# Optimization experiments

Hardware: AMD Instinct MI355X
Metric: run time of the kernel (lower is better)

## Reference

```python
import jax, jax.numpy as jnp
import numpy as np


def setup_inputs() -> dict:
    key = jax.random.key(0)
    kq, kk, kv = jax.random.split(key, 3)
    d_head, sq, skv = 128, 8192, 8192
    q = jax.random.normal(kq, (d_head, sq), dtype=jnp.float32)
    k = jax.random.normal(kk, (d_head, skv), dtype=jnp.float32)
    v = jax.random.normal(kv, (d_head, skv), dtype=jnp.float32)
    return {"q": q, "k": k, "v": v}


def reference(q, k, v):
    # qk: (seqlen_q, seqlen_kv) -- full score matrix, no 1/sqrt(d) scaling (faithful)
    qk = jnp.einsum('dq,dk->qk', q, k)
    row_max = jnp.max(qk, axis=1, keepdims=True)
    exp_row = jnp.exp(qk - row_max)
    scores = exp_row / jnp.sum(exp_row, axis=1, keepdims=True)
    # attn_out: (seqlen_q, d_head)
    attn_out = jnp.einsum('qk,dk->qd', scores, v)
    return attn_out
```

## Files before the change

### kernel.cpp

```cpp
#include <hip/hip_runtime.h>
#include <hip/hip_bf16.h>
#include <math.h>

typedef _Float16 half8 __attribute__((ext_vector_type(8)));
typedef __fp16 fp16x2 __attribute__((ext_vector_type(2)));
typedef float f32x4 __attribute__((ext_vector_type(4)));
typedef float f32x16 __attribute__((ext_vector_type(16)));
typedef unsigned uint4v __attribute__((ext_vector_type(4)));

#define D 128
#define SQ 8192
#define SKV 8192
#define BQ 256
#define BKV 64
#define LOG2E 1.4426950408889634f
#define DEFER_THR 11.5417f

__device__ __forceinline__ float bf2f(ushort h) {
  union { unsigned u; float f; } v; v.u = ((unsigned)h) << 16;
  return v.f;
}
__device__ __forceinline__ unsigned cvtpk_bf(float a, float b) {
  unsigned r;
  asm("v_cvt_pk_bf16_f32 %0, %1, %2" : "=v"(r) : "v"(a), "v"(b));
  return r;
}
__device__ __forceinline__ unsigned cvtpk_h(float a, float b) {
  union { fp16x2 h; unsigned u; } r;
  r.h = __builtin_amdgcn_cvt_pkrtz(a, b);
  return r.u;
}
__device__ __forceinline__ float fexp2(float x) {
  float r;
  asm("v_exp_f32 %0, %1" : "=v"(r) : "v"(x));
  return r;
}
__device__ __forceinline__ float fmax3(float a, float b, float c) {
  float r;
  asm("v_max3_f32 %0, %1, %2, %3" : "=v"(r) : "v"(a), "v"(b), "v"(c));
  return r;
}
__device__ __forceinline__ void pl32swap(unsigned& a, unsigned& b) {
  asm("v_permlane32_swap_b32 %0, %1" : "+v"(a), "+v"(b));
}

__global__ void prep_all(const float* __restrict__ q, const float* __restrict__ k,
                         const float* __restrict__ v,
                         _Float16* __restrict__ QT, _Float16* __restrict__ PK,
                         _Float16* __restrict__ PV) {
  int b = blockIdx.x;
  int t = threadIdx.x;
  if (b < 512) {
    const bool isQ = (b < 256);
    const float* src = isQ ? q : k;
    const float scl = isQ ? LOG2E : 1.0f;
    int s0 = (isQ ? b : b - 256) * 32;
    __shared__ float lds[128][33];
    int dr = t >> 5, l = t & 31;
#pragma unroll
    for (int j = 0; j < 16; ++j) {
      int dd = dr * 16 + j;
      lds[dd][l] = src[(size_t)dd * SQ + s0 + l];
    }
    __syncthreads();
#pragma unroll
    for (int i = 0; i < 2; ++i) {
      int cid = t + i * 256;
      int c = cid >> 5, sl = cid & 31;
      half8 hv;
#pragma unroll
      for (int e = 0; e < 8; ++e) hv[e] = (_Float16)(lds[c * 8 + e][sl] * scl);
      if (isQ) {
        *(half8*)(QT + (size_t)(s0 + sl) * D + c * 8) = hv;
      } else {
        int srow = s0 + sl;
        size_t elem = (size_t)((srow >> 5) * 8 + (c >> 1)) * 512 +
                      ((c & 1) * 32 + (srow & 31)) * 8;
        *(half8*)(PK + elem) = hv;
      }
    }
  } else {
    int idx = (b - 512) * 256 + t;
    int i8 = idx * 8;
    float4 x0 = *(const float4*)(v + i8);
    float4 x1 = *(const float4*)(v + i8 + 4);
    int drow = i8 >> 13;
    int kv = i8 & (SKV - 1);
    size_t elem = (size_t)(kv >> 6) * 8192 +
                  (size_t)((drow >> 5) * 4 + ((kv >> 4) & 3)) * 512 +
                  (((kv >> 3) & 1) * 32 + (drow & 31)) * 8;
    half8 hv = { (_Float16)x0.x, (_Float16)x0.y, (_Float16)x0.z, (_Float16)x0.w,
                 (_Float16)x1.x, (_Float16)x1.y, (_Float16)x1.z, (_Float16)x1.w };
    *(half8*)(PV + elem) = hv;
  }
}

__global__ __launch_bounds__(512, 2)
void flash_fwd(const _Float16* __restrict__ QT, const _Float16* __restrict__ PK,
               const _Float16* __restrict__ PV,
               ushort* __restrict__ Opart, float* __restrict__ Mst,
               float* __restrict__ Lst, int splitLen) {
  __shared__ _Float16 Kl[2][BKV * D];
  __shared__ _Float16 Vl[3][BKV * D];

  const int tid = threadIdx.x;
  const int w = tid >> 6;
  const int lane = tid & 63;
  const int lc = lane & 31;
  const int hi = lane >> 5;
  const int qb = blockIdx.x;
  const int split = blockIdx.y;
  const int qrow = qb * BQ + w * 32 + lc;

  half8 qh[8];
#pragma unroll
  for (int ds = 0; ds < 8; ++ds)
    qh[ds] = *(const half8*)(QT + (size_t)qrow * D + ds * 16 + hi * 8);

  f32x16 Ot[4];
#pragma unroll
  for (int dt = 0; dt < 4; ++dt)
#pragma unroll
    for (int e = 0; e < 16; ++e) Ot[dt][e] = 0.f;
  float mrun = -INFINITY, lrun = 0.f;

  const int kvBase = split * splitLen;
  const int nsteps = splitLen / BKV;
  const int tB = kvBase / BKV;

#define STAGE(KB, VB, T)                                                      \
  {                                                                           \
    _Pragma("unroll")                                                         \
    for (int j = 0; j < 4; ++j) {                                             \
      int cblk = w * 4 + j;                                                   \
      int cc = cblk & 15;                                                     \
      const _Float16* gp = ((cblk < 16) ? PK : PV) +                          \
                           (size_t)(T) * (BKV * D) + cc * 512 + lane * 8;     \
      _Float16* lp = ((cblk < 16) ? &Kl[KB][0] : &Vl[VB][0]) + cc * 512;      \
      __builtin_amdgcn_global_load_lds(                                       \
          (const __attribute__((address_space(1))) unsigned*)gp,              \
          (__attribute__((address_space(3))) unsigned*)lp, 16, 0, 0);         \
    }                                                                         \
  }

  auto QKX = [&](int kb2, f32x16& s0, f32x16& s1) {
    const _Float16* kb = &Kl[kb2][0] + lane * 8;
#pragma unroll
    for (int e = 0; e < 16; ++e) { s0[e] = 0.f; s1[e] = 0.f; }
    __builtin_amdgcn_s_setprio(1);
#pragma unroll
    for (int ds = 0; ds < 8; ++ds) {
      half8 k0 = *(const half8*)(kb + ds * 512);
      half8 k1 = *(const half8*)(kb + (8 + ds) * 512);
      s0 = __builtin_amdgcn_mfma_f32_32x32x16_f16(k0, qh[ds], s0, 0, 0, 0);
      s1 = __builtin_amdgcn_mfma_f32_32x32x16_f16(k1, qh[ds], s1, 0, 0, 0);
    }
    __builtin_amdgcn_s_setprio(0);
  };

  auto SMPV = [&](f32x16& s0, f32x16& s1, int vb3) {
    const _Float16* vb = &Vl[vb3][0] + lane * 8;
    half8 va[16];
#pragma unroll
    for (int f = 0; f < 16; ++f) va[f] = *(const half8*)(vb + f * 512);

    float m0 = fmax3(s0[0], s0[1], s0[2]);
    float m1 = fmax3(s0[3], s0[4], s0[5]);
    float m2 = fmax3(s0[6], s0[7], s0[8]);
    float m3 = fmax3(s0[9], s0[10], s0[11]);
    float m4 = fmax3(s0[12], s0[13], s0[14]);
    float m5 = fmax3(s0[15], s1[0], s1[1]);
    float m6 = fmax3(s1[2], s1[3], s1[4]);
    float m7 = fmax3(s1[5], s1[6], s1[7]);
    float m8 = fmax3(s1[8], s1[9], s1[10]);
    float m9 = fmax3(s1[11], s1[12], s1[13]);
    float ma = fmaxf(s1[14], s1[15]);
    float n0 = fmax3(m0, m1, m2);
    float n1 = fmax3(m3, m4, m5);
    float n2 = fmax3(m6, m7, m8);
    float n3 = fmaxf(m9, ma);
    float mx = fmaxf(fmax3(n0, n1, n2), n3);
    mx = fmaxf(mx, __shfl_xor(mx, 32));

    if (!__all(mx - mrun <= DEFER_THR)) {
      float mn = fmaxf(mrun, mx);
      float sc = fexp2(mrun - mn);
      mrun = mn;
      lrun *= sc;
#pragma unroll
      for (int dt = 0; dt < 4; ++dt)
#pragma unroll
        for (int e = 0; e < 16; ++e) Ot[dt][e] *= sc;
    }
#pragma unroll
    for (int e = 0; e < 16; ++e) {
      s0[e] = fexp2(s0[e] - mrun);
      s1[e] = fexp2(s1[e] - mrun);
    }
    float a8[8];
#pragma unroll
    for (int e = 0; e < 8; ++e) a8[e] = (s0[e] + s0[e + 8]) + (s1[e] + s1[e + 8]);
    float lsum = ((a8[0] + a8[4]) + (a8[1] + a8[5])) +
                 ((a8[2] + a8[6]) + (a8[3] + a8[7]));
    lsum += __shfl_xor(lsum, 32);
    lrun += lsum;

    unsigned pk[8];
    half8 pb[4];
    union { unsigned u[4]; half8 v; } pbu;
#pragma unroll
    for (int j = 0; j < 8; ++j) pk[j] = cvtpk_h(s0[2 * j], s0[2 * j + 1]);
    pl32swap(pk[0], pk[2]); pl32swap(pk[1], pk[3]);
    pl32swap(pk[4], pk[6]); pl32swap(pk[5], pk[7]);
    pbu.u[0] = pk[0]; pbu.u[1] = pk[1]; pbu.u[2] = pk[2]; pbu.u[3] = pk[3]; pb[0] = pbu.v;
    pbu.u[0] = pk[4]; pbu.u[1] = pk[5]; pbu.u[2] = pk[6]; pbu.u[3] = pk[7]; pb[1] = pbu.v;
#pragma unroll
    for (int j = 0; j < 8; ++j) pk[j] = cvtpk_h(s1[2 * j], s1[2 * j + 1]);
    pl32swap(pk[0], pk[2]); pl32swap(pk[1], pk[3]);
    pl32swap(pk[4], pk[6]); pl32swap(pk[5], pk[7]);
    pbu.u[0] = pk[0]; pbu.u[1] = pk[1]; pbu.u[2] = pk[2]; pbu.u[3] = pk[3]; pb[2] = pbu.v;
    pbu.u[0] = pk[4]; pbu.u[1] = pk[5]; pbu.u[2] = pk[6]; pbu.u[3] = pk[7]; pb[3] = pbu.v;

    __builtin_amdgcn_s_setprio(1);
#pragma unroll
    for (int dt = 0; dt < 4; ++dt) {
      Ot[dt] = __builtin_amdgcn_mfma_f32_32x32x16_f16(va[dt * 4 + 0], pb[0], Ot[dt], 0, 0, 0);
      Ot[dt] = __builtin_amdgcn_mfma_f32_32x32x16_f16(va[dt * 4 + 1], pb[1], Ot[dt], 0, 0, 0);
      Ot[dt] = __builtin_amdgcn_mfma_f32_32x32x16_f16(va[dt * 4 + 2], pb[2], Ot[dt], 0, 0, 0);
      Ot[dt] = __builtin_amdgcn_mfma_f32_32x32x16_f16(va[dt * 4 + 3], pb[3], Ot[dt], 0, 0, 0);
    }
    __builtin_amdgcn_s_setprio(0);
  };

  f32x16 sA0, sA1, sB0, sB1;

  STAGE(0, 0, tB);
  __syncthreads();
  if (nsteps > 1) STAGE(1, 1, tB + 1);
  QKX(0, sA0, sA1);
  __syncthreads();

  int p = 1;
  for (; p + 1 < nsteps; p += 2) {
    STAGE(0, (p + 1) % 3, tB + p + 1);
    QKX(1, sB0, sB1);
    SMPV(sA0, sA1, (p - 1) % 3);
    __syncthreads();
    if (p + 2 < nsteps) STAGE(1, (p + 2) % 3, tB + p + 2);
    QKX(0, sA0, sA1);
    SMPV(sB0, sB1, p % 3);
    __syncthreads();
  }
  if (p < nsteps) {
    QKX(1, sB0, sB1);
    SMPV(sA0, sA1, (p - 1) % 3);
    SMPV(sB0, sB1, p % 3);
  } else {
    SMPV(sA0, sA1, (nsteps - 1) % 3);
  }

  ushort* Op = Opart + (size_t)split * SQ * D + (size_t)qrow * D;
#pragma unroll
  for (int dt = 0; dt < 4; ++dt) {
#pragma unroll
    for (int rg = 0; rg < 4; ++rg) {
      uint2 o2;
      o2.x = cvtpk_bf(Ot[dt][4 * rg + 0], Ot[dt][4 * rg + 1]);
      o2.y = cvtpk_bf(Ot[dt][4 * rg + 2], Ot[dt][4 * rg + 3]);
      *(uint2*)(Op + dt * 32 + rg * 8 + hi * 4) = o2;
    }
  }
  if (hi == 0) {
    Mst[split * SQ + qrow] = mrun;
    Lst[split * SQ + qrow] = lrun;
  }
}

__global__ void combine(const ushort* __restrict__ Opart, const float* __restrict__ Mst,
                        const float* __restrict__ Lst, float* __restrict__ out, int nsplit) {
  int t8 = (blockIdx.x * 256 + threadIdx.x) * 8;
  int qi = t8 >> 7;
  float M = -INFINITY;
  for (int s = 0; s < nsplit; ++s) M = fmaxf(M, Mst[s * SQ + qi]);
  float acc[8] = {0.f, 0.f, 0.f, 0.f, 0.f, 0.f, 0.f, 0.f};
  float den = 0.f;
  for (int s = 0; s < nsplit; ++s) {
    float wgt = fexp2(Mst[s * SQ + qi] - M);
    den += wgt * Lst[s * SQ + qi];
    uint4v u = *(const uint4v*)(Opart + (size_t)s * SQ * D + t8);
#pragma unroll
    for (int j = 0; j < 4; ++j) {
      acc[2 * j]     += wgt * bf2f((ushort)(u[j] & 0xffffu));
      acc[2 * j + 1] += wgt * bf2f((ushort)(u[j] >> 16));
    }
  }
  float inv = 1.0f / den;
  f32x4 o0 = { acc[0] * inv, acc[1] * inv, acc[2] * inv, acc[3] * inv };
  f32x4 o1 = { acc[4] * inv, acc[5] * inv, acc[6] * inv, acc[7] * inv };
  *(f32x4*)(out + t8) = o0;
  *(f32x4*)(out + t8 + 4) = o1;
}

extern "C" void kernel_launch(void* const* d_in, const int* in_sizes, int n_in,
                              void* d_out, int out_size, void* d_ws, size_t ws_size,
                              hipStream_t stream) {
  const float* q = (const float*)d_in[0];
  const float* k = (const float*)d_in[1];
  const float* v = (const float*)d_in[2];
  float* out = (float*)d_out;

  char* ws = (char*)d_ws;
  const size_t mat = (size_t)SQ * D * 2;
  _Float16* QT = (_Float16*)(ws);
  _Float16* PK = (_Float16*)(ws + mat);
  _Float16* PV = (_Float16*)(ws + 2 * mat);
  char* rest = ws + 3 * mat;

  const size_t opartSz = (size_t)SQ * D * 2;
  const size_t statSz  = (size_t)SQ * 4;
  int nsplit = 8;
  while (nsplit > 1 &&
         3 * mat + (size_t)nsplit * (opartSz + 2 * statSz) > ws_size) nsplit >>= 1;

  ushort* Opart = (ushort*)rest;
  float* Mst = (float*)(rest + (size_t)nsplit * opartSz);
  float* Lst = (float*)(rest + (size_t)nsplit * opartSz + (size_t)nsplit * statSz);

  prep_all<<<1024, 256, 0, stream>>>(q, k, v, QT, PK, PV);
  flash_fwd<<<dim3(SQ / BQ, nsplit), 512, 0, stream>>>(QT, PK, PV,
                                                       Opart, Mst, Lst, SKV / nsplit);
  combine<<<(SQ * D) / (256 * 8), 256, 0, stream>>>(Opart, Mst, Lst, out, nsplit);
}
```

Baseline: 57.75 us.

## Interleave QK MFMA chunks with softmax stages of previous tile

After: 58.73 us. No clear change (+1.7%).

```diff
diff --git a/kernel.cpp b/kernel.cpp
--- a/kernel.cpp
+++ b/kernel.cpp
@@ -143,18 +143,26 @@
     }                                                                         \
   }
 
+#define QKCHUNK(kb, d0, s0, s1)                                               \
+  {                                                                           \
+    _Pragma("unroll")                                                         \
+    for (int ds = (d0); ds < (d0) + 2; ++ds) {                                \
+      half8 k0 = *(const half8*)(kb + ds * 512);                              \
+      half8 k1 = *(const half8*)(kb + (8 + ds) * 512);                        \
+      s0 = __builtin_amdgcn_mfma_f32_32x32x16_f16(k0, qh[ds], s0, 0, 0, 0);   \
+      s1 = __builtin_amdgcn_mfma_f32_32x32x16_f16(k1, qh[ds], s1, 0, 0, 0);   \
+    }                                                                         \
+  }
+
   auto QKX = [&](int kb2, f32x16& s0, f32x16& s1) {
     const _Float16* kb = &Kl[kb2][0] + lane * 8;
 #pragma unroll
     for (int e = 0; e < 16; ++e) { s0[e] = 0.f; s1[e] = 0.f; }
     __builtin_amdgcn_s_setprio(1);
-#pragma unroll
-    for (int ds = 0; ds < 8; ++ds) {
-      half8 k0 = *(const half8*)(kb + ds * 512);
-      half8 k1 = *(const half8*)(kb + (8 + ds) * 512);
-      s0 = __builtin_amdgcn_mfma_f32_32x32x16_f16(k0, qh[ds], s0, 0, 0, 0);
-      s1 = __builtin_amdgcn_mfma_f32_32x32x16_f16(k1, qh[ds], s1, 0, 0, 0);
-    }
+    QKCHUNK(kb, 0, s0, s1);
+    QKCHUNK(kb, 2, s0, s1);
+    QKCHUNK(kb, 4, s0, s1);
+    QKCHUNK(kb, 6, s0, s1);
     __builtin_amdgcn_s_setprio(0);
   };
 
@@ -163,7 +171,6 @@
     half8 va[16];
 #pragma unroll
     for (int f = 0; f < 16; ++f) va[f] = *(const half8*)(vb + f * 512);
-
     float m0 = fmax3(s0[0], s0[1], s0[2]);
     float m1 = fmax3(s0[3], s0[4], s0[5]);
     float m2 = fmax3(s0[6], s0[7], s0[8]);
@@ -175,13 +182,9 @@
     float m8 = fmax3(s1[8], s1[9], s1[10]);
     float m9 = fmax3(s1[11], s1[12], s1[13]);
     float ma = fmaxf(s1[14], s1[15]);
-    float n0 = fmax3(m0, m1, m2);
-    float n1 = fmax3(m3, m4, m5);
-    float n2 = fmax3(m6, m7, m8);
-    float n3 = fmaxf(m9, ma);
-    float mx = fmaxf(fmax3(n0, n1, n2), n3);
+    float mx = fmaxf(fmax3(fmax3(m0, m1, m2), fmax3(m3, m4, m5),
+                           fmax3(m6, m7, m8)), fmax3(m9, ma, ma));
     mx = fmaxf(mx, __shfl_xor(mx, 32));
-
     if (!__all(mx - mrun <= DEFER_THR)) {
       float mn = fmaxf(mrun, mx);
       float sc = fexp2(mrun - mn);
@@ -204,7 +207,6 @@
                  ((a8[2] + a8[6]) + (a8[3] + a8[7]));
     lsum += __shfl_xor(lsum, 32);
     lrun += lsum;
-
     unsigned pk[8];
     half8 pb[4];
     union { unsigned u[4]; half8 v; } pbu;
@@ -220,7 +222,6 @@
     pl32swap(pk[4], pk[6]); pl32swap(pk[5], pk[7]);
     pbu.u[0] = pk[0]; pbu.u[1] = pk[1]; pbu.u[2] = pk[2]; pbu.u[3] = pk[3]; pb[2] = pbu.v;
     pbu.u[0] = pk[4]; pbu.u[1] = pk[5]; pbu.u[2] = pk[6]; pbu.u[3] = pk[7]; pb[3] = pbu.v;
-
     __builtin_amdgcn_s_setprio(1);
 #pragma unroll
     for (int dt = 0; dt < 4; ++dt) {
@@ -232,6 +233,98 @@
     __builtin_amdgcn_s_setprio(0);
   };
 
+  auto PHASE = [&](int kbN, f32x16& sN0, f32x16& sN1,
+                   f32x16& sP0, f32x16& sP1, int vbP) {
+    const _Float16* kb = &Kl[kbN][0] + lane * 8;
+    const _Float16* vb = &Vl[vbP][0] + lane * 8;
+    half8 va[16];
+#pragma unroll
+    for (int f = 0; f < 16; ++f) va[f] = *(const half8*)(vb + f * 512);
+#pragma unroll
+    for (int e = 0; e < 16; ++e) { sN0[e] = 0.f; sN1[e] = 0.f; }
+
+    __builtin_amdgcn_s_setprio(1);
+    QKCHUNK(kb, 0, sN0, sN1);
+    __builtin_amdgcn_s_setprio(0);
+    {
+      float m0 = fmax3(sP0[0], sP0[1], sP0[2]);
+      float m1 = fmax3(sP0[3], sP0[4], sP0[5]);
+      float m2 = fmax3(sP0[6], sP0[7], sP0[8]);
+      float m3 = fmax3(sP0[9], sP0[10], sP0[11]);
+      float m4 = fmax3(sP0[12], sP0[13], sP0[14]);
+      float m5 = fmax3(sP0[15], sP1[0], sP1[1]);
+      float m6 = fmax3(sP1[2], sP1[3], sP1[4]);
+      float m7 = fmax3(sP1[5], sP1[6], sP1[7]);
+      float m8 = fmax3(sP1[8], sP1[9], sP1[10]);
+      float m9 = fmax3(sP1[11], sP1[12], sP1[13]);
+      float ma = fmaxf(sP1[14], sP1[15]);
+      float mx = fmaxf(fmax3(fmax3(m0, m1, m2), fmax3(m3, m4, m5),
+                             fmax3(m6, m7, m8)), fmax3(m9, ma, ma));
+      mx = fmaxf(mx, __shfl_xor(mx, 32));
+      if (!__all(mx - mrun <= DEFER_THR)) {
+        float mn = fmaxf(mrun, mx);
+        float sc = fexp2(mrun - mn);
+        mrun = mn;
+        lrun *= sc;
+#pragma unroll
+        for (int dt = 0; dt < 4; ++dt)
+#pragma unroll
+          for (int e = 0; e < 16; ++e) Ot[dt][e] *= sc;
+      }
+    }
+
+    __builtin_amdgcn_s_setprio(1);
+    QKCHUNK(kb, 2, sN0, sN1);
+    __builtin_amdgcn_s_setprio(0);
+    {
+#pragma unroll
+      for (int e = 0; e < 16; ++e) {
+        sP0[e] = fexp2(sP0[e] - mrun);
+        sP1[e] = fexp2(sP1[e] - mrun);
+      }
+      float a8[8];
+#pragma unroll
+      for (int e = 0; e < 8; ++e)
+        a8[e] = (sP0[e] + sP0[e + 8]) + (sP1[e] + sP1[e + 8]);
+      float lsum = ((a8[0] + a8[4]) + (a8[1] + a8[5])) +
+                   ((a8[2] + a8[6]) + (a8[3] + a8[7]));
+      lsum += __shfl_xor(lsum, 32);
+      lrun += lsum;
+    }
+
+    half8 pb[4];
+    __builtin_amdgcn_s_setprio(1);
+    QKCHUNK(kb, 4, sN0, sN1);
+    __builtin_amdgcn_s_setprio(0);
+    {
+      unsigned pk[8];
+      union { unsigned u[4]; half8 v; } pbu;
+#pragma unroll
+      for (int j = 0; j < 8; ++j) pk[j] = cvtpk_h(sP0[2 * j], sP0[2 * j + 1]);
+      pl32swap(pk[0], pk[2]); pl32swap(pk[1], pk[3]);
+      pl32swap(pk[4], pk[6]); pl32swap(pk[5], pk[7]);
+      pbu.u[0] = pk[0]; pbu.u[1] = pk[1]; pbu.u[2] = pk[2]; pbu.u[3] = pk[3]; pb[0] = pbu.v;
+      pbu.u[0] = pk[4]; pbu.u[1] = pk[5]; pbu.u[2] = pk[6]; pbu.u[3] = pk[7]; pb[1] = pbu.v;
+#pragma unroll
+      for (int j = 0; j < 8; ++j) pk[j] = cvtpk_h(sP1[2 * j], sP1[2 * j + 1]);
+      pl32swap(pk[0], pk[2]); pl32swap(pk[1], pk[3]);
+      pl32swap(pk[4], pk[6]); pl32swap(pk[5], pk[7]);
+      pbu.u[0] = pk[0]; pbu.u[1] = pk[1]; pbu.u[2] = pk[2]; pbu.u[3] = pk[3]; pb[2] = pbu.v;
+      pbu.u[0] = pk[4]; pbu.u[1] = pk[5]; pbu.u[2] = pk[6]; pbu.u[3] = pk[7]; pb[3] = pbu.v;
+    }
+
+    __builtin_amdgcn_s_setprio(1);
+    QKCHUNK(kb, 6, sN0, sN1);
+#pragma unroll
+    for (int dt = 0; dt < 4; ++dt) {
+      Ot[dt] = __builtin_amdgcn_mfma_f32_32x32x16_f16(va[dt * 4 + 0], pb[0], Ot[dt], 0, 0, 0);
+      Ot[dt] = __builtin_amdgcn_mfma_f32_32x32x16_f16(va[dt * 4 + 1], pb[1], Ot[dt], 0, 0, 0);
+      Ot[dt] = __builtin_amdgcn_mfma_f32_32x32x16_f16(va[dt * 4 + 2], pb[2], Ot[dt], 0, 0, 0);
+      Ot[dt] = __builtin_amdgcn_mfma_f32_32x32x16_f16(va[dt * 4 + 3], pb[3], Ot[dt], 0, 0, 0);
+    }
+    __builtin_amdgcn_s_setprio(0);
+  };
+
   f32x16 sA0, sA1, sB0, sB1;
 
   STAGE(0, 0, tB);
@@ -243,17 +336,14 @@
   int p = 1;
   for (; p + 1 < nsteps; p += 2) {
     STAGE(0, (p + 1) % 3, tB + p + 1);
-    QKX(1, sB0, sB1);
-    SMPV(sA0, sA1, (p - 1) % 3);
+    PHASE(1, sB0, sB1, sA0, sA1, (p - 1) % 3);
     __syncthreads();
     if (p + 2 < nsteps) STAGE(1, (p + 2) % 3, tB + p + 2);
-    QKX(0, sA0, sA1);
-    SMPV(sB0, sB1, p % 3);
+    PHASE(0, sA0, sA1, sB0, sB1, p % 3);
     __syncthreads();
   }
   if (p < nsteps) {
-    QKX(1, sB0, sB1);
-    SMPV(sA0, sA1, (p - 1) % 3);
+    PHASE(1, sB0, sB1, sA0, sA1, (p - 1) % 3);
     SMPV(sB0, sB1, p % 3);
   } else {
     SMPV(sA0, sA1, (nsteps - 1) % 3);
```
